# Kernel optimization log

Measured on AMD Instinct MI355X. Metric: run time of the kernel, lower is better.

The kernel has to match this reference:

```python
import jax, jax.numpy as jnp
import numpy as np

N_NODES = 50000
NEG_SLOPE = 0.2


def setup_inputs() -> dict:
    key = jax.random.key(0)
    ks = jax.random.split(key, 10)
    d = {
        'x': jax.random.normal(ks[0], (N_NODES, 128), dtype=jnp.float32),
        'edge_index': jax.random.randint(ks[1], (2, 800000), 0, N_NODES, dtype=jnp.int64),
        'W1': jax.random.normal(ks[2], (128, 512), dtype=jnp.float32) * (1.0 / np.sqrt(128)),
        'att_src1': jax.random.normal(ks[3], (8, 64), dtype=jnp.float32) * 0.1,
        'att_dst1': jax.random.normal(ks[4], (8, 64), dtype=jnp.float32) * 0.1,
        'b1': jax.random.normal(ks[5], (512,), dtype=jnp.float32) * 0.02,
        'W2': jax.random.normal(ks[6], (512, 1), dtype=jnp.float32) * (1.0 / np.sqrt(512)),
        'att_src2': jax.random.normal(ks[7], (1, 1), dtype=jnp.float32) * 0.1,
        'att_dst2': jax.random.normal(ks[8], (1, 1), dtype=jnp.float32) * 0.1,
        'b2': jax.random.normal(ks[9], (1,), dtype=jnp.float32) * 0.02,
    }
    return d


def _gat_layer(x, src, dst, W, a_src, a_dst, b):
    # x: [N, F_in]; W: [F_in, H*C]; a_src/a_dst: [H, C]; b: [H*C]
    N = x.shape[0]
    H, C = a_src.shape
    xh = (x @ W).reshape(N, H, C)                      # [N, H, C]
    s = jnp.sum(xh * a_src, axis=-1)                   # [N, H] source logits
    t = jnp.sum(xh * a_dst, axis=-1)                   # [N, H] target logits
    e = s[src] + t[dst]                                # [E, H]
    e = jnp.where(e > 0, e, NEG_SLOPE * e)             # leaky_relu(0.2)
    emax = jax.ops.segment_max(e, dst, num_segments=N)  # per-target max (self-loops guarantee coverage)
    ex = jnp.exp(e - emax[dst])                        # [E, H]
    denom = jax.ops.segment_sum(ex, dst, num_segments=N)  # [N, H]
    alpha = ex / denom[dst]                            # softmax over incoming edges
    msg = xh[src] * alpha[:, :, None]                  # [E, H, C]
    out = jax.ops.segment_sum(msg, dst, num_segments=N)   # [N, H, C]
    return out.reshape(N, H * C) + b


def reference(x, edge_index, W1, att_src1, att_dst1, b1, W2, att_src2, att_dst2, b2):
    N = x.shape[0]
    # add self-loops (PyG GATConv default)
    loop = jnp.arange(N, dtype=edge_index.dtype)
    src = jnp.concatenate([edge_index[0], loop])
    dst = jnp.concatenate([edge_index[1], loop])
    h = _gat_layer(x, src, dst, W1, att_src1, att_dst1, b1)   # [N, 512]
    h = jax.nn.relu(h)
    out = _gat_layer(h, src, dst, W2, att_src2, att_dst2, b2)  # [N, 1]
    return out.reshape(-1)
```

## Files before the change

kernel.cpp:

```cpp
#include <hip/hip_runtime.h>
#include <math.h>

#define NEG_SLOPE 0.2f

typedef __attribute__((ext_vector_type(8))) short bf16x8;
typedef __attribute__((ext_vector_type(4))) float f32x4;

__device__ __forceinline__ float leaky(float v){ return v > 0.f ? v : NEG_SLOPE * v; }

static __device__ __forceinline__ unsigned int f2bf(float x){
  unsigned u = __float_as_uint(x);
  return (u + 0x7fffu + ((u >> 16) & 1u)) >> 16;
}

__global__ void k_prep0(const float* __restrict__ W1, const float* __restrict__ as,
                        const float* __restrict__ ad, float* __restrict__ wst,
                        bf16x8* __restrict__ packh,
                        const int* __restrict__ dst, int E, int* __restrict__ deg){
  int b = blockIdx.x, t = threadIdx.x;
  if (b == 0){
    int k = t & 127, half = t >> 7;
    const float* a = half ? ad : as;
    for (int h = 0; h < 8; ++h){
      float sum = 0.f;
      for (int c = 0; c < 64; ++c) sum += W1[(size_t)k * 512 + h * 64 + c] * a[h * 64 + c];
      wst[k * 16 + half * 8 + h] = sum;
    }
  } else if (b < 33){
    int g = (b - 1) * 256 + t;
    int lane = g & 63, kt = (g >> 6) & 3, ctl = (g >> 8) & 3, h = g >> 10;
    int gc = h * 64 + ctl * 16 + (lane & 15);
    int k0 = kt * 32 + (lane >> 4) * 8;
    bf16x8 hv;
    #pragma unroll
    for (int i = 0; i < 8; ++i)
      hv[i] = (short)f2bf(W1[(size_t)(k0 + i) * 512 + gc]);
    packh[g] = hv;
  } else {
    int i = (b - 33) * 256 + t;
    if (i < E) atomicAdd(&deg[dst[i]], 1);
  }
}

__global__ void k_scan1(const int* __restrict__ deg, int* __restrict__ tmp,
                        int* __restrict__ bsum, int N){
  __shared__ int ws[4];
  int tid = threadIdx.x;
  int i = blockIdx.x * 256 + tid;
  int v = (i < N) ? deg[i] : 0;
  int lane = tid & 63, wv = tid >> 6;
  int x = v;
  #pragma unroll
  for (int off = 1; off < 64; off <<= 1){
    int y = __shfl_up(x, off, 64);
    if (lane >= off) x += y;
  }
  if (lane == 63) ws[wv] = x;
  __syncthreads();
  int p = 0;
  for (int w = 0; w < wv; ++w) p += ws[w];
  x += p;
  if (i < N) tmp[i] = x;
  if (tid == 255) bsum[blockIdx.x] = x;
}

__global__ void k_scan2(int* __restrict__ bsum, int nb){
  __shared__ int ws[4];
  int tid = threadIdx.x;
  int v = (tid < nb) ? bsum[tid] : 0;
  int lane = tid & 63, wv = tid >> 6;
  int x = v;
  #pragma unroll
  for (int off = 1; off < 64; off <<= 1){
    int y = __shfl_up(x, off, 64);
    if (lane >= off) x += y;
  }
  if (lane == 63) ws[wv] = x;
  __syncthreads();
  int p = 0;
  for (int w = 0; w < wv; ++w) p += ws[w];
  x += p;
  if (tid < nb) bsum[tid] = x;
}

__device__ __forceinline__ int rp_of(int j, const int* __restrict__ tmp,
                                     const int* __restrict__ bsum){
  if (j == 0) return 0;
  int i = j - 1, blk = i >> 8;
  return tmp[i] + (blk ? bsum[blk - 1] : 0);
}

__global__ void k_fill3(const int* __restrict__ src, const int* __restrict__ dst, int E,
                        const int* __restrict__ tmp, const int* __restrict__ bsum,
                        int* __restrict__ rowptr, int* __restrict__ fill,
                        int* __restrict__ esrc, int N){
  int i = blockIdx.x * blockDim.x + threadIdx.x;
  if (i <= N) rowptr[i] = rp_of(i, tmp, bsum);
  if (i < E){
    int d = dst[i];
    int row0 = rp_of(d, tmp, bsum);
    int pos = row0 + atomicAdd(&fill[d], 1);
    esrc[pos] = src[i];
  }
}

__global__ __launch_bounds__(256) void k_logits_xb(const float* __restrict__ x,
                                                   const float* __restrict__ wst,
                                                   float* __restrict__ s, float* __restrict__ t,
                                                   unsigned int* __restrict__ xb, int N){
  __shared__ float xs[64][132];
  __shared__ float wl[2048];
  int tid = threadIdx.x;
  int n0 = blockIdx.x * 64;
  for (int i = tid; i < 2048; i += 256) wl[i] = wst[i];
  for (int i = tid; i < 2048; i += 256){
    int r = i >> 5, c4 = (i & 31) << 2;
    float4 v = make_float4(0.f, 0.f, 0.f, 0.f);
    if (n0 + r < N) v = *(const float4*)(x + (size_t)(n0 + r) * 128 + c4);
    xs[r][c4 + 0] = v.x; xs[r][c4 + 1] = v.y; xs[r][c4 + 2] = v.z; xs[r][c4 + 3] = v.w;
  }
  __syncthreads();
  int node = tid & 63, og = tid >> 6;
  int o = og * 4;
  float a0 = 0.f, a1 = 0.f, a2 = 0.f, a3 = 0.f;
  for (int k = 0; k < 128; ++k){
    float v = xs[node][k];
    a0 += v * wl[k * 16 + o + 0];
    a1 += v * wl[k * 16 + o + 1];
    a2 += v * wl[k * 16 + o + 2];
    a3 += v * wl[k * 16 + o + 3];
  }
  int n = n0 + node;
  if (n < N){
    if (o < 8){
      s[n * 8 + o + 0] = a0; s[n * 8 + o + 1] = a1;
      s[n * 8 + o + 2] = a2; s[n * 8 + o + 3] = a3;
    } else {
      int oo = o - 8;
      t[n * 8 + oo + 0] = a0; t[n * 8 + oo + 1] = a1;
      t[n * 8 + oo + 2] = a2; t[n * 8 + oo + 3] = a3;
    }
  }
  for (int i = tid; i < 4096; i += 256){
    int r = i >> 6, j = i & 63;
    int n2 = n0 + r;
    if (n2 < N)
      xb[(size_t)n2 * 64 + j] = f2bf(xs[r][2 * j]) | (f2bf(xs[r][2 * j + 1]) << 16);
  }
}

__global__ __launch_bounds__(512, 8) void k_agg_gemm(
    const unsigned int* __restrict__ xb,
    const float* __restrict__ s, const float* __restrict__ t,
    const int* __restrict__ rowptr, const int* __restrict__ esrc,
    const bf16x8* __restrict__ packh,
    const float* __restrict__ b1, const float* __restrict__ W2,
    float* __restrict__ xh2, int N)
{
  __shared__ unsigned int ylds[8192];
  __shared__ float lal[8][128];
  __shared__ float red[8][16];
  int tid = threadIdx.x;
  int w = tid >> 6, lane = tid & 63;
  int m0 = blockIdx.x * 16;
  int h = lane & 7;
  int es = lane >> 3;

  for (int ni = 0; ni < 2; ++ni){
    int nl = w * 2 + ni;
    int n = m0 + nl;
    float acc[16];
    #pragma unroll
    for (int i = 0; i < 16; ++i) acc[i] = 0.f;

    if (n < N){
      int row0 = rowptr[n], deg = rowptr[n + 1] - row0;
      float tn = t[(size_t)n * 8 + h];
      float sn = s[(size_t)n * 8 + h];
      float selfe = __expf(leaky(sn + tn));

      {
        unsigned int v = xb[(size_t)n * 64 + lane];
        float f0 = __uint_as_float(v << 16);
        float f1 = __uint_as_float(v & 0xffff0000u);
        #pragma unroll
        for (int hh = 0; hh < 8; ++hh){
          float a = __shfl(selfe, hh, 64);
          acc[2 * hh]     += a * f0;
          acc[2 * hh + 1] += a * f1;
        }
      }
      float dsum = (lane < 8) ? selfe : 0.f;

      float* lb = lal[w];
      for (int base = 0; base < deg; base += 8){
        float* la = lb + ((base >> 3) & 1) * 64;
        int e = base + es;
        int cnt = min(8, deg - base);
        int srcl = 0;
        if (e < deg) srcl = esrc[row0 + e];
        float sv = s[(size_t)srcl * 8 + h];
        int sj[8];
        #pragma unroll
        for (int j = 0; j < 8; ++j) sj[j] = __shfl(srcl, j << 3, 64);
        unsigned int vv[8];
        #pragma unroll
        for (int j = 0; j < 8; ++j) vv[j] = xb[(size_t)sj[j] * 64 + lane];
        float ev = (e < deg) ? __expf(leaky(sv + tn)) : 0.f;
        dsum += ev;
        la[lane] = ev;
        #pragma unroll
        for (int j = 0; j < 8; ++j){
          if (j < cnt){
            float4 q0 = *(float4*)&la[j * 8];
            float4 q1 = *(float4*)&la[j * 8 + 4];
            float f0 = __uint_as_float(vv[j] << 16);
            float f1 = __uint_as_float(vv[j] & 0xffff0000u);
            acc[0]  += q0.x * f0; acc[1]  += q0.x * f1;
            acc[2]  += q0.y * f0; acc[3]  += q0.y * f1;
            acc[4]  += q0.z * f0; acc[5]  += q0.z * f1;
            acc[6]  += q0.w * f0; acc[7]  += q0.w * f1;
            acc[8]  += q1.x * f0; acc[9]  += q1.x * f1;
            acc[10] += q1.y * f0; acc[11] += q1.y * f1;
            acc[12] += q1.z * f0; acc[13] += q1.z * f1;
            acc[14] += q1.w * f0; acc[15] += q1.w * f1;
          }
        }
      }

      dsum += __shfl_xor(dsum, 8, 64);
      dsum += __shfl_xor(dsum, 16, 64);
      dsum += __shfl_xor(dsum, 32, 64);
      float iden = 1.f / dsum;
      #pragma unroll
      for (int hh = 0; hh < 8; ++hh){
        float a = __shfl(iden, hh, 64);
        acc[2 * hh]     *= a;
        acc[2 * hh + 1] *= a;
      }
    }

    #pragma unroll
    for (int hh = 0; hh < 8; ++hh){
      unsigned int p = f2bf(acc[2 * hh]) | (f2bf(acc[2 * hh + 1]) << 16);
      unsigned int byte = (unsigned)(nl * 2048 + hh * 256 + lane * 4);
      byte ^= (unsigned)((nl & 7) << 4);
      ylds[byte >> 2] = p;
    }
  }
  __syncthreads();

  int lr = lane & 15, lg = lane >> 4;
  int hD = w;
  float pnode[4] = {0.f, 0.f, 0.f, 0.f};
  bf16x8 A[4];
  #pragma unroll
  for (int kt = 0; kt < 4; ++kt){
    unsigned int byte = (unsigned)(lr * 2048 + hD * 256 + kt * 64 + lg * 16);
    byte ^= (unsigned)((lr & 7) << 4);
    A[kt] = *(const bf16x8*)((const char*)ylds + byte);
  }
  #pragma unroll
  for (int ctl = 0; ctl < 4; ++ctl){
    f32x4 acc2 = {0.f, 0.f, 0.f, 0.f};
    int pb = ((hD * 4 + ctl) * 4) * 64 + lane;
    #pragma unroll
    for (int kt = 0; kt < 4; ++kt)
      acc2 = __builtin_amdgcn_mfma_f32_16x16x32_bf16(A[kt], packh[pb + kt * 64], acc2, 0, 0, 0);
    int gc = hD * 64 + ctl * 16 + lr;
    float bb = b1[gc], wv = W2[gc];
    #pragma unroll
    for (int r = 0; r < 4; ++r){
      float o = acc2[r] + bb; o = o > 0.f ? o : 0.f;
      pnode[r] += o * wv;
    }
  }
  #pragma unroll
  for (int r = 0; r < 4; ++r){
    float v = pnode[r];
    v += __shfl_xor(v, 1, 64);
    v += __shfl_xor(v, 2, 64);
    v += __shfl_xor(v, 4, 64);
    v += __shfl_xor(v, 8, 64);
    pnode[r] = v;
  }
  if (lr == 0){
    #pragma unroll
    for (int r = 0; r < 4; ++r) red[w][lg * 4 + r] = pnode[r];
  }
  __syncthreads();
  if (tid < 16){
    int node = m0 + tid;
    if (node < N){
      float sum = 0.f;
      #pragma unroll
      for (int ww = 0; ww < 8; ++ww) sum += red[ww][tid];
      xh2[node] = sum;
    }
  }
}

__global__ void k_agg2(const float* __restrict__ xh2, const int* __restrict__ rowptr,
                       const int* __restrict__ esrc,
                       const float* __restrict__ as2p, const float* __restrict__ ad2p,
                       const float* __restrict__ b2p,
                       float* __restrict__ out, int N)
{
  int n = blockIdx.x * blockDim.x + threadIdx.x;
  if (n >= N) return;
  float a_s = as2p[0], a_d = ad2p[0], b2 = b2p[0];
  float xn = xh2[n];
  float t2 = a_d * xn;
  float w0 = __expf(leaky(a_s * xn + t2));
  float den = w0, num = w0 * xn;
  int row1 = rowptr[n + 1];
  for (int e = rowptr[n]; e < row1; ++e){
    int src = esrc[e];
    float xs2 = xh2[src];
    float w = __expf(leaky(a_s * xs2 + t2));
    den += w; num += w * xs2;
  }
  out[n] = num / den + b2;
}

extern "C" void kernel_launch(void* const* d_in, const int* in_sizes, int n_in,
                              void* d_out, int out_size, void* d_ws, size_t ws_size,
                              hipStream_t stream) {
  const float* x   = (const float*)d_in[0];
  const int*   ei  = (const int*)d_in[1];
  const float* W1  = (const float*)d_in[2];
  const float* as1 = (const float*)d_in[3];
  const float* ad1 = (const float*)d_in[4];
  const float* b1  = (const float*)d_in[5];
  const float* W2  = (const float*)d_in[6];
  const float* as2 = (const float*)d_in[7];
  const float* ad2 = (const float*)d_in[8];
  const float* b2  = (const float*)d_in[9];
  float* out = (float*)d_out;

  int N = in_sizes[0] / 128;
  int E = in_sizes[1] / 2;
  const int* src_in = ei;
  const int* dst_in = ei + E;

  char* w = (char*)d_ws;
  auto alloc = [&](size_t bytes){ void* p = (void*)w; w += (bytes + 255) & ~(size_t)255; return p; };
  unsigned int* xb   = (unsigned int*)alloc((size_t)N * 64 * 4);
  float* s      = (float*)alloc((size_t)N * 8 * 4);
  float* t      = (float*)alloc((size_t)N * 8 * 4);
  float* xh2    = (float*)alloc((size_t)N * 4);
  int*   cnts   = (int*)alloc((size_t)2 * N * 4);
  int*   deg    = cnts;
  int*   fill   = cnts + N;
  int*   rowptr = (int*)alloc((size_t)(N + 1) * 4);
  int*   esrc   = (int*)alloc((size_t)E * 4);
  int*   tmp    = (int*)alloc((size_t)N * 4);
  int*   bsum   = (int*)alloc((size_t)1024 * 4);
  float* wst    = (float*)alloc((size_t)2048 * 4);
  bf16x8* packh = (bf16x8*)alloc((size_t)8192 * 16);

  int nb = (N + 255) / 256;

  hipMemsetAsync(cnts, 0, (size_t)2 * N * 4, stream);
  k_prep0<<<33 + (E + 255) / 256, 256, 0, stream>>>(W1, as1, ad1, wst, packh, dst_in, E, deg);
  k_logits_xb<<<(N + 63) / 64, 256, 0, stream>>>(x, wst, s, t, xb, N);
  k_scan1<<<nb, 256, 0, stream>>>(deg, tmp, bsum, N);
  k_scan2<<<1, 256, 0, stream>>>(bsum, nb);
  k_fill3<<<(E + 255) / 256, 256, 0, stream>>>(src_in, dst_in, E, tmp, bsum, rowptr, fill, esrc, N);
  k_agg_gemm<<<(N + 15) / 16, 512, 0, stream>>>(xb, s, t, rowptr, esrc, packh, b1, W2, xh2, N);
  k_agg2<<<(N + 255) / 256, 256, 0, stream>>>(xh2, rowptr, esrc, as2, ad2, b2, out, N);
}
```

Measured before the change: 199.6 us.

## Fuse block-sum scan into fill, prefetch edge sources, parallelize layer-2 aggregation

Removes the single-block scan kernel by having every fill block redo the small block-sum scan in shared memory, and reorders launches so CSR construction comes before the logits kernel. The layer-1 aggregation loop now prefetches the next chunk's source indices and logits and drops the per-edge count guard, relying on zero-weight padding. Layer-2 aggregation uses 8 lanes per node with shuffle reductions instead of one thread per node. The logits kernel gets vectorized float4 weight loads and a different shared-memory padding. Each fill block repeats a redundant scan, and nb must stay at or below 256.

Result: slower. 289.0 us (+44.8%).

```diff
diff --git a/kernel.cpp b/kernel.cpp
--- a/kernel.cpp
+++ b/kernel.cpp
@@ -64,41 +64,41 @@
   if (tid == 255) bsum[blockIdx.x] = x;
 }
 
-__global__ void k_scan2(int* __restrict__ bsum, int nb){
+__global__ __launch_bounds__(256) void k_fill3(const int* __restrict__ src,
+                        const int* __restrict__ dst, int E,
+                        const int* __restrict__ tmp, const int* __restrict__ bsumraw,
+                        int* __restrict__ rowptr, int* __restrict__ fill,
+                        int* __restrict__ esrc, int N, int nb){
+  __shared__ int bs[256];
   __shared__ int ws[4];
   int tid = threadIdx.x;
-  int v = (tid < nb) ? bsum[tid] : 0;
-  int lane = tid & 63, wv = tid >> 6;
-  int x = v;
-  #pragma unroll
-  for (int off = 1; off < 64; off <<= 1){
-    int y = __shfl_up(x, off, 64);
-    if (lane >= off) x += y;
-  }
-  if (lane == 63) ws[wv] = x;
-  __syncthreads();
-  int p = 0;
-  for (int w = 0; w < wv; ++w) p += ws[w];
-  x += p;
-  if (tid < nb) bsum[tid] = x;
-}
-
-__device__ __forceinline__ int rp_of(int j, const int* __restrict__ tmp,
-                                     const int* __restrict__ bsum){
-  if (j == 0) return 0;
-  int i = j - 1, blk = i >> 8;
-  return tmp[i] + (blk ? bsum[blk - 1] : 0);
-}
-
-__global__ void k_fill3(const int* __restrict__ src, const int* __restrict__ dst, int E,
-                        const int* __restrict__ tmp, const int* __restrict__ bsum,
-                        int* __restrict__ rowptr, int* __restrict__ fill,
-                        int* __restrict__ esrc, int N){
-  int i = blockIdx.x * blockDim.x + threadIdx.x;
-  if (i <= N) rowptr[i] = rp_of(i, tmp, bsum);
+  {
+    int v = (tid < nb) ? bsumraw[tid] : 0;
+    int lane = tid & 63, wv = tid >> 6;
+    int x = v;
+    #pragma unroll
+    for (int off = 1; off < 64; off <<= 1){
+      int y = __shfl_up(x, off, 64);
+      if (lane >= off) x += y;
+    }
+    if (lane == 63) ws[wv] = x;
+    __syncthreads();
+    int p = 0;
+    for (int w = 0; w < wv; ++w) p += ws[w];
+    bs[tid] = x + p;
+    __syncthreads();
+  }
+  int i = blockIdx.x * 256 + tid;
+  if (i <= N){
+    int r;
+    if (i == 0) r = 0;
+    else { int ii = i - 1, blk = ii >> 8; r = tmp[ii] + (blk ? bs[blk - 1] : 0); }
+    rowptr[i] = r;
+  }
   if (i < E){
     int d = dst[i];
-    int row0 = rp_of(d, tmp, bsum);
+    int ii = d - 1, blk = ii >> 8;
+    int row0 = (d == 0) ? 0 : tmp[ii] + (blk ? bs[blk - 1] : 0);
     int pos = row0 + atomicAdd(&fill[d], 1);
     esrc[pos] = src[i];
   }
@@ -108,7 +108,7 @@
                                                    const float* __restrict__ wst,
                                                    float* __restrict__ s, float* __restrict__ t,
                                                    unsigned int* __restrict__ xb, int N){
-  __shared__ float xs[64][132];
+  __shared__ float xs[64][133];
   __shared__ float wl[2048];
   int tid = threadIdx.x;
   int n0 = blockIdx.x * 64;
@@ -125,10 +125,11 @@
   float a0 = 0.f, a1 = 0.f, a2 = 0.f, a3 = 0.f;
   for (int k = 0; k < 128; ++k){
     float v = xs[node][k];
-    a0 += v * wl[k * 16 + o + 0];
-    a1 += v * wl[k * 16 + o + 1];
-    a2 += v * wl[k * 16 + o + 2];
-    a3 += v * wl[k * 16 + o + 3];
+    float4 wv4 = *(const float4*)&wl[k * 16 + o];
+    a0 += v * wv4.x;
+    a1 += v * wv4.y;
+    a2 += v * wv4.z;
+    a3 += v * wv4.w;
   }
   int n = n0 + node;
   if (n < N){
@@ -193,39 +194,46 @@
       float dsum = (lane < 8) ? selfe : 0.f;
 
       float* lb = lal[w];
-      for (int base = 0; base < deg; base += 8){
-        float* la = lb + ((base >> 3) & 1) * 64;
-        int e = base + es;
-        int cnt = min(8, deg - base);
-        int srcl = 0;
-        if (e < deg) srcl = esrc[row0 + e];
-        float sv = s[(size_t)srcl * 8 + h];
+      int nch = (deg + 7) >> 3;
+      int srcl_c = 0; float sv_c = 0.f;
+      if (nch > 0){
+        srcl_c = (es < deg) ? esrc[row0 + es] : 0;
+        sv_c = s[(size_t)srcl_c * 8 + h];
+      }
+      for (int c = 0; c < nch; ++c){
+        int srcl_n = 0; float sv_n = 0.f;
+        if (c + 1 < nch){
+          int e = (c + 1) * 8 + es;
+          srcl_n = (e < deg) ? esrc[row0 + e] : 0;
+          sv_n = s[(size_t)srcl_n * 8 + h];
+        }
         int sj[8];
         #pragma unroll
-        for (int j = 0; j < 8; ++j) sj[j] = __shfl(srcl, j << 3, 64);
+        for (int j = 0; j < 8; ++j) sj[j] = __shfl(srcl_c, j << 3, 64);
         unsigned int vv[8];
         #pragma unroll
         for (int j = 0; j < 8; ++j) vv[j] = xb[(size_t)sj[j] * 64 + lane];
-        float ev = (e < deg) ? __expf(leaky(sv + tn)) : 0.f;
+        int e = c * 8 + es;
+        float ev = (e < deg) ? __expf(leaky(sv_c + tn)) : 0.f;
         dsum += ev;
+        float* la = lb + ((c & 1) << 6);
         la[lane] = ev;
         #pragma unroll
         for (int j = 0; j < 8; ++j){
-          if (j < cnt){
-            float4 q0 = *(float4*)&la[j * 8];
-            float4 q1 = *(float4*)&la[j * 8 + 4];
-            float f0 = __uint_as_float(vv[j] << 16);
-            float f1 = __uint_as_float(vv[j] & 0xffff0000u);
-            acc[0]  += q0.x * f0; acc[1]  += q0.x * f1;
-            acc[2]  += q0.y * f0; acc[3]  += q0.y * f1;
-            acc[4]  += q0.z * f0; acc[5]  += q0.z * f1;
-            acc[6]  += q0.w * f0; acc[7]  += q0.w * f1;
-            acc[8]  += q1.x * f0; acc[9]  += q1.x * f1;
-            acc[10] += q1.y * f0; acc[11] += q1.y * f1;
-            acc[12] += q1.z * f0; acc[13] += q1.z * f1;
-            acc[14] += q1.w * f0; acc[15] += q1.w * f1;
-          }
+          float4 q0 = *(float4*)&la[j * 8];
+          float4 q1 = *(float4*)&la[j * 8 + 4];
+          float f0 = __uint_as_float(vv[j] << 16);
+          float f1 = __uint_as_float(vv[j] & 0xffff0000u);
+          acc[0]  += q0.x * f0; acc[1]  += q0.x * f1;
+          acc[2]  += q0.y * f0; acc[3]  += q0.y * f1;
+          acc[4]  += q0.z * f0; acc[5]  += q0.z * f1;
+          acc[6]  += q0.w * f0; acc[7]  += q0.w * f1;
+          acc[8]  += q1.x * f0; acc[9]  += q1.x * f1;
+          acc[10] += q1.y * f0; acc[11] += q1.y * f1;
+          acc[12] += q1.z * f0; acc[13] += q1.z * f1;
+          acc[14] += q1.w * f0; acc[15] += q1.w * f1;
         }
+        srcl_c = srcl_n; sv_c = sv_n;
       }
 
       dsum += __shfl_xor(dsum, 8, 64);
@@ -300,27 +308,34 @@
   }
 }
 
-__global__ void k_agg2(const float* __restrict__ xh2, const int* __restrict__ rowptr,
-                       const int* __restrict__ esrc,
+__global__ __launch_bounds__(256) void k_agg2(const float* __restrict__ xh2,
+                       const int* __restrict__ rowptr, const int* __restrict__ esrc,
                        const float* __restrict__ as2p, const float* __restrict__ ad2p,
                        const float* __restrict__ b2p,
                        float* __restrict__ out, int N)
 {
-  int n = blockIdx.x * blockDim.x + threadIdx.x;
-  if (n >= N) return;
+  int g = blockIdx.x * 32 + (threadIdx.x >> 3);
+  int li = threadIdx.x & 7;
+  if (g >= N) return;
   float a_s = as2p[0], a_d = ad2p[0], b2 = b2p[0];
-  float xn = xh2[n];
+  float xn = xh2[g];
   float t2 = a_d * xn;
-  float w0 = __expf(leaky(a_s * xn + t2));
-  float den = w0, num = w0 * xn;
-  int row1 = rowptr[n + 1];
-  for (int e = rowptr[n]; e < row1; ++e){
+  float den = 0.f, num = 0.f;
+  if (li == 0){
+    float w0 = __expf(leaky(a_s * xn + t2));
+    den = w0; num = w0 * xn;
+  }
+  int row1 = rowptr[g + 1];
+  for (int e = rowptr[g] + li; e < row1; e += 8){
     int src = esrc[e];
     float xs2 = xh2[src];
     float w = __expf(leaky(a_s * xs2 + t2));
     den += w; num += w * xs2;
   }
-  out[n] = num / den + b2;
+  den += __shfl_xor(den, 1, 64); num += __shfl_xor(num, 1, 64);
+  den += __shfl_xor(den, 2, 64); num += __shfl_xor(num, 2, 64);
+  den += __shfl_xor(den, 4, 64); num += __shfl_xor(num, 4, 64);
+  if (li == 0) out[g] = num / den + b2;
 }
 
 extern "C" void kernel_launch(void* const* d_in, const int* in_sizes, int n_in,
@@ -363,10 +378,9 @@
 
   hipMemsetAsync(cnts, 0, (size_t)2 * N * 4, stream);
   k_prep0<<<33 + (E + 255) / 256, 256, 0, stream>>>(W1, as1, ad1, wst, packh, dst_in, E, deg);
+  k_scan1<<<nb, 256, 0, stream>>>(deg, tmp, bsum, N);
+  k_fill3<<<(E + 255) / 256, 256, 0, stream>>>(src_in, dst_in, E, tmp, bsum, rowptr, fill, esrc, N, nb);
   k_logits_xb<<<(N + 63) / 64, 256, 0, stream>>>(x, wst, s, t, xb, N);
-  k_scan1<<<nb, 256, 0, stream>>>(deg, tmp, bsum, N);
-  k_scan2<<<1, 256, 0, stream>>>(bsum, nb);
-  k_fill3<<<(E + 255) / 256, 256, 0, stream>>>(src_in, dst_in, E, tmp, bsum, rowptr, fill, esrc, N);
   k_agg_gemm<<<(N + 15) / 16, 512, 0, stream>>>(xb, s, t, rowptr, esrc, packh, b1, W2, xh2, N);
-  k_agg2<<<(N + 255) / 256, 256, 0, stream>>>(xh2, rowptr, esrc, as2, ad2, b2, out, N);
-}
+  k_agg2<<<(N + 31) / 32, 256, 0, stream>>>(xh2, rowptr, esrc, as2, ad2, b2, out, N);
+}
```
